# Performance work log

Hardware: AMD Instinct MI355X
Metric: run time of the kernel (lower is better)

## Reference

```python
import jax, jax.numpy as jnp
import numpy as np

KS = 3          # kernel size (forced by the view() shape constraint)
STRIDE = 1
PAD = 1
DIL = 1
K = KS * KS     # 9 taps


def _bilinear_sample(x, py, px):
    """x: [B,C,Hin,Win]; py,px: [B,C,K,H,W] float sample coords.
    Zero padding outside bounds (torchvision DeformConv semantics:
    each corner contributes only if it lies inside the image)."""
    B, C, Hin, Win = x.shape
    y0 = jnp.floor(py)
    x0 = jnp.floor(px)
    wy1 = py - y0
    wx1 = px - x0
    wy0 = 1.0 - wy1
    wx0 = 1.0 - wx1
    xf = x.reshape(B, C, Hin * Win)

    def gather(yi, xi):
        valid = (yi >= 0) & (yi <= Hin - 1) & (xi >= 0) & (xi <= Win - 1)
        yc = jnp.clip(yi, 0, Hin - 1).astype(jnp.int32)
        xc = jnp.clip(xi, 0, Win - 1).astype(jnp.int32)
        flat = (yc * Win + xc).reshape(B, C, -1)
        g = jnp.take_along_axis(xf, flat, axis=2).reshape(yi.shape)
        return jnp.where(valid, g, 0.0)

    return (wy0 * wx0 * gather(y0, x0)
            + wy0 * wx1 * gather(y0, x0 + 1)
            + wy1 * wx0 * gather(y0 + 1, x0)
            + wy1 * wx1 * gather(y0 + 1, x0 + 1))


def setup_inputs() -> dict:
    key = jax.random.key(0)
    ks = jax.random.split(key, 5)
    B, C, H, W = 8, 64, 128, 128
    Cout = 64
    return {
        "x": jax.random.normal(ks[0], (B, C, H, W), dtype=jnp.float32),
        # depthwise offset conv: groups=C, out = 18*C -> weight (18C, 1, 3, 3)
        "offset_w": jax.random.normal(ks[1], (2 * K * C, 1, 3, 3), dtype=jnp.float32) * 0.05,
        "offset_b": jax.random.normal(ks[2], (2 * K * C,), dtype=jnp.float32) * 0.05,
        "deform_w": jax.random.normal(ks[3], (Cout, C, KS, KS), dtype=jnp.float32) * 0.05,
        "deform_b": jax.random.normal(ks[4], (Cout,), dtype=jnp.float32) * 0.05,
    }


def reference(x, offset_w, offset_b, deform_w, deform_b):
    B, C, H, W = x.shape
    Cout = deform_w.shape[0]

    # 1) depthwise offset conv (groups = in_channels)
    off = jax.lax.conv_general_dilated(
        x, offset_w, window_strides=(STRIDE, STRIDE),
        padding=((PAD, PAD), (PAD, PAD)), rhs_dilation=(DIL, DIL),
        feature_group_count=C,
        dimension_numbers=("NCHW", "OIHW", "NCHW"))
    off = off + offset_b[None, :, None, None]

    # 2) softmax over the full channel axis (dim=1 in torch)
    off = jax.nn.softmax(off, axis=1)

    # 3) torchvision offset layout: channel 2*(g*K + k) + {0:dy, 1:dx},
    #    deformable_groups = C (per-input-channel offsets)
    off = off.reshape(B, C, K, 2, H, W)
    dy = off[:, :, :, 0]   # [B,C,K,H,W]
    dx = off[:, :, :, 1]

    base_y = (jnp.arange(H, dtype=x.dtype) * STRIDE - PAD)   # [H]
    base_x = (jnp.arange(W, dtype=x.dtype) * STRIDE - PAD)   # [W]
    ky = (jnp.repeat(jnp.arange(KS), KS) * DIL).astype(x.dtype)  # [K]
    kx = (jnp.tile(jnp.arange(KS), KS) * DIL).astype(x.dtype)

    py = base_y[None, None, None, :, None] + ky[None, None, :, None, None] + dy
    px = base_x[None, None, None, None, :] + kx[None, None, :, None, None] + dx

    sampled = _bilinear_sample(x, py, px)                    # [B,C,K,H,W]

    # 4) weighted accumulation over (c_in, kernel tap)
    out = jnp.einsum("bckhw,ock->bohw", sampled, deform_w.reshape(Cout, C, K))
    return out + deform_b[None, :, None, None]
```

## Files before the change

kernel.cpp:

```cpp
#include <hip/hip_runtime.h>

#define B_    8
#define C_    64
#define H_    128
#define W_    128
#define K_    9
#define J_    18
#define COUT_ 64
#define TPX   16
#define CK    576
#define SROW  584

typedef __attribute__((ext_vector_type(8))) short short8;
typedef __attribute__((ext_vector_type(4))) float float4v;

__device__ __forceinline__ unsigned short f2bf(float f) {
    unsigned int u = __float_as_uint(f);
    u = u + 0x7fffu + ((u >> 16) & 1u);
    return (unsigned short)(u >> 16);
}

constexpr int TMAP[9] = {0, 1, 2, 7, 8, 9, 14, 15, 16};

__global__ __launch_bounds__(256)
void nchw_to_nhwc(const float* __restrict__ x, float* __restrict__ xt) {
    __shared__ float tile[64][65];
    const int bid = blockIdx.x;
    const int wt  = bid & 1;
    const int h   = (bid >> 1) & 127;
    const int b   = bid >> 8;
    const int w0  = wt << 6;
    const int q   = threadIdx.x >> 6;
    const int l   = threadIdx.x & 63;
    #pragma unroll
    for (int r = 0; r < 16; r++) {
        const int c = q * 16 + r;
        tile[c][l] = x[((size_t)(b * C_ + c) * H_ + h) * W_ + w0 + l];
    }
    __syncthreads();
    #pragma unroll
    for (int r = 0; r < 16; r++) {
        const int w = q * 16 + r;
        xt[((size_t)(b * H_ + h) * W_ + w0 + w) * C_ + l] = tile[l][w];
    }
}

__global__ __launch_bounds__(256)
void conv_dw_bf16(const float* __restrict__ dw, unsigned short* __restrict__ dwb) {
    const int i = blockIdx.x * 256 + threadIdx.x;
    if (i < CK * COUT_) dwb[i] = f2bf(dw[i]);
}

template<int T>
__device__ __forceinline__ void conv_steps(const unsigned int* __restrict__ owc,
                                           const float (&S)[28], float (&v)[4][J_]) {
    if constexpr (T < 81) {
        const unsigned int pw = owc[T];
        const float wlo = __uint_as_float(pw << 16);
        const float whi = __uint_as_float(pw & 0xffff0000u);
        constexpr int e0 = 2 * T, e1 = 2 * T + 1;
        constexpr int j0 = e0 / 9, p0 = TMAP[e0 % 9];
        constexpr int j1 = e1 / 9, p1 = TMAP[e1 % 9];
        #pragma unroll
        for (int px = 0; px < 4; px++) {
            v[px][j0] = fmaf(wlo, S[p0 + px], v[px][j0]);
            v[px][j1] = fmaf(whi, S[p1 + px], v[px][j1]);
        }
        conv_steps<T + 1>(owc, S, v);
    }
}

template<int I>
__device__ __forceinline__ void finish_px(float (&v)[J_], const float (&S)[28],
                                          unsigned short* __restrict__ sb) {
    float sum = 0.0f;
    #pragma unroll
    for (int j = 0; j < J_; j++) { v[j] = __expf(v[j]); sum += v[j]; }
    #pragma unroll
    for (int off = 32; off >= 1; off >>= 1) sum += __shfl_xor(sum, off, 64);
    const float inv = 1.0f / sum;
    #pragma unroll
    for (int k = 0; k < K_; k++) {
        const float dy = v[2 * k] * inv;
        const float dx = v[2 * k + 1] * inv;
        const int base = TMAP[k] + I;
        const float a  = S[base],     bb = S[base + 1];
        const float c  = S[base + 7], dd = S[base + 8];
        const float top = a + dx * (bb - a);
        const float bot = c + dx * (dd - c);
        sb[k] = f2bf(top + dy * (bot - top));
    }
}

template<bool NHWC, bool PREB>
__global__ __launch_bounds__(256, 3)
void dcn_fused(const float* __restrict__ xsrc,
               const float* __restrict__ ow,
               const float* __restrict__ ob,
               const float* __restrict__ dw,
               const unsigned short* __restrict__ dwb,
               const float* __restrict__ db,
               float* __restrict__ out) {
    __shared__ unsigned int ow_s[C_ * 81];
    __shared__ __align__(16) unsigned short sbuf[TPX * SROW];

    const int tid  = threadIdx.x;
    const int wave = tid >> 6;
    const int lane = tid & 63;

    const int bid = blockIdx.x;
    const int b   = bid >> 10;
    const int rem = bid & 1023;
    const int h   = rem >> 3;
    const int w0  = (rem & 7) << 4;

    const float2* ow2 = (const float2*)ow;
    for (int i = tid; i < C_ * 81; i += 256) {
        float2 f = ow2[i];
        ow_s[i] = (unsigned int)f2bf(f.x) | ((unsigned int)f2bf(f.y) << 16);
    }

    __syncthreads();

    const int wbase = w0 + (wave << 2);
    const unsigned int* owc = ow_s + lane * 81;
    const float2* obp = (const float2*)(ob + lane * J_);

    float S[28];
    #pragma unroll
    for (int r = 0; r < 4; r++) {
        const int y = h - 1 + r;
        const bool yv = (unsigned)y < (unsigned)H_;
        #pragma unroll
        for (int s = 0; s < 7; s++) {
            const int xx = wbase - 1 + s;
            const bool ok = yv && ((unsigned)xx < (unsigned)W_);
            float val;
            if (NHWC) {
                const float* p = xsrc + ((size_t)(b * H_ + (y & 127)) * W_ + (xx & 127)) * C_ + lane;
                val = ok ? *p : 0.0f;
            } else {
                const float* p = xsrc + ((size_t)(b * C_ + lane) * H_ + (y & 127)) * W_ + (xx & 127);
                val = ok ? *p : 0.0f;
            }
            S[r * 7 + s] = val;
        }
    }

    float v[4][J_];
    #pragma unroll
    for (int p = 0; p < 9; p++) {
        const float2 f = obp[p];
        #pragma unroll
        for (int px = 0; px < 4; px++) { v[px][2 * p] = f.x; v[px][2 * p + 1] = f.y; }
    }
    conv_steps<0>(owc, S, v);

    unsigned short* sb = sbuf + (wave << 2) * SROW + lane * K_;
    finish_px<0>(v[0], S, sb);
    finish_px<1>(v[1], S, sb + SROW);
    finish_px<2>(v[2], S, sb + 2 * SROW);
    finish_px<3>(v[3], S, sb + 3 * SROW);

    __syncthreads();

    const int quad = lane >> 4;
    const int o    = (wave << 4) + (lane & 15);
    float4v acc = {0.f, 0.f, 0.f, 0.f};
    const unsigned short* arow = sbuf + (lane & 15) * SROW + quad * 8;
    #pragma unroll
    for (int t = 0; t < 18; t++) {
        short8 afrag = *(const short8*)(arow + t * 32);
        short8 bfrag;
        if (PREB) {
            bfrag = *(const short8*)(dwb + (size_t)o * CK + quad * 8 + t * 32);
        } else {
            const float* brow = dw + (size_t)o * CK + quad * 8 + t * 32;
            float4 b0 = *(const float4*)brow;
            float4 b1 = *(const float4*)(brow + 4);
            union { short8 s8; unsigned short u[8]; } bfu;
            bfu.u[0] = f2bf(b0.x); bfu.u[1] = f2bf(b0.y); bfu.u[2] = f2bf(b0.z); bfu.u[3] = f2bf(b0.w);
            bfu.u[4] = f2bf(b1.x); bfu.u[5] = f2bf(b1.y); bfu.u[6] = f2bf(b1.z); bfu.u[7] = f2bf(b1.w);
            bfrag = bfu.s8;
        }
        acc = __builtin_amdgcn_mfma_f32_16x16x32_bf16(afrag, bfrag, acc, 0, 0, 0);
    }
    const float bias = db[o];
    const int px0 = quad << 2;
    float4 res;
    res.x = acc[0] + bias; res.y = acc[1] + bias; res.z = acc[2] + bias; res.w = acc[3] + bias;
    *(float4*)(out + ((size_t)(b * COUT_ + o) * H_ + h) * W_ + w0 + px0) = res;
}

extern "C" void kernel_launch(void* const* d_in, const int* in_sizes, int n_in,
                              void* d_out, int out_size, void* d_ws, size_t ws_size,
                              hipStream_t stream) {
    (void)in_sizes; (void)n_in; (void)out_size;
    const float* x  = (const float*)d_in[0];
    const float* ow = (const float*)d_in[1];
    const float* ob = (const float*)d_in[2];
    const float* dw = (const float*)d_in[3];
    const float* db = (const float*)d_in[4];
    float* outp = (float*)d_out;

    const size_t xbytes  = (size_t)B_ * C_ * H_ * W_ * sizeof(float);
    const size_t dwbytes = (size_t)CK * COUT_ * sizeof(unsigned short);
    const dim3 grid(B_ * H_ * (W_ / TPX)), blk(256);

    if (ws_size >= xbytes + dwbytes) {
        float* xt = (float*)d_ws;
        unsigned short* dwb = (unsigned short*)((char*)d_ws + xbytes);
        nchw_to_nhwc<<<dim3(B_ * H_ * (W_ / 64)), blk, 0, stream>>>(x, xt);
        conv_dw_bf16<<<dim3((CK * COUT_ + 255) / 256), blk, 0, stream>>>(dw, dwb);
        dcn_fused<true, true><<<grid, blk, 0, stream>>>(xt, ow, ob, dw, dwb, db, outp);
    } else if (ws_size >= xbytes) {
        float* xt = (float*)d_ws;
        nchw_to_nhwc<<<dim3(B_ * H_ * (W_ / 64)), blk, 0, stream>>>(x, xt);
        dcn_fused<true, false><<<grid, blk, 0, stream>>>(xt, ow, ob, dw, nullptr, db, outp);
    } else {
        dcn_fused<false, false><<<grid, blk, 0, stream>>>(x, ow, ob, dw, nullptr, db, outp);
    }
}
```

Measured before the change: 206.0 us.

## Prepack offset weights, alias LDS buffers, use packed FMA and exp2 softmax

Offset-conv weights are now repacked once in a prep kernel into a dy/dx-paired bf16 layout, pre-scaled by log2(e), so each block copies them into LDS instead of converting them. The shared weight buffer and the bf16 tap buffer now alias one LDS allocation, which cuts LDS per block and may allow more resident blocks. The offset conv uses packed two-wide FMAs, exp becomes exp2, and the reciprocal uses the hardware rcp. The cross-lane sum uses ds_swizzle for four pixels at once, and a fast path skips bounds checks for interior windows. It adds a barrier before the LDS reuse and slightly less accurate exp and reciprocal.

```diff
diff --git a/kernel.cpp b/kernel.cpp
--- a/kernel.cpp
+++ b/kernel.cpp
@@ -10,9 +10,12 @@
 #define TPX   16
 #define CK    576
 #define SROW  584
+#define NW81  (C_ * 81)
+#define L2E   1.4426950408889634f
 
 typedef __attribute__((ext_vector_type(8))) short short8;
 typedef __attribute__((ext_vector_type(4))) float float4v;
+typedef __attribute__((ext_vector_type(2))) float f32x2;
 
 __device__ __forceinline__ unsigned short f2bf(float f) {
     unsigned int u = __float_as_uint(f);
@@ -46,63 +49,74 @@
 }
 
 __global__ __launch_bounds__(256)
-void conv_dw_bf16(const float* __restrict__ dw, unsigned short* __restrict__ dwb) {
-    const int i = blockIdx.x * 256 + threadIdx.x;
-    if (i < CK * COUT_) dwb[i] = f2bf(dw[i]);
+void prep_weights(const float* __restrict__ dw, unsigned short* __restrict__ dwb,
+                  const float* __restrict__ ow, unsigned int* __restrict__ owp) {
+    const int bid = blockIdx.x;
+    const int dwblocks = (CK * COUT_) / 256;
+    if (bid < dwblocks) {
+        const int i = bid * 256 + threadIdx.x;
+        dwb[i] = f2bf(dw[i]);
+    } else {
+        const int i = (bid - dwblocks) * 256 + threadIdx.x;
+        if (i < NW81) {
+            const int c = i / 81, r = i - c * 81;
+            const int k = r / 9,  t = r - k * 9;
+            const float* s = ow + c * 162 + k * 18 + t;
+            owp[i] = (unsigned int)f2bf(s[0] * L2E) |
+                     ((unsigned int)f2bf(s[9] * L2E) << 16);
+        }
+    }
 }
 
 template<int T>
 __device__ __forceinline__ void conv_steps(const unsigned int* __restrict__ owc,
-                                           const float (&S)[28], float (&v)[4][J_]) {
+                                           const float (&S)[28], f32x2 (&v2)[4][9]) {
     if constexpr (T < 81) {
         const unsigned int pw = owc[T];
-        const float wlo = __uint_as_float(pw << 16);
-        const float whi = __uint_as_float(pw & 0xffff0000u);
-        constexpr int e0 = 2 * T, e1 = 2 * T + 1;
-        constexpr int j0 = e0 / 9, p0 = TMAP[e0 % 9];
-        constexpr int j1 = e1 / 9, p1 = TMAP[e1 % 9];
+        const f32x2 w2 = {__uint_as_float(pw << 16),
+                          __uint_as_float(pw & 0xffff0000u)};
+        constexpr int k = T / 9;
+        constexpr int p = TMAP[T % 9];
         #pragma unroll
         for (int px = 0; px < 4; px++) {
-            v[px][j0] = fmaf(wlo, S[p0 + px], v[px][j0]);
-            v[px][j1] = fmaf(whi, S[p1 + px], v[px][j1]);
-        }
-        conv_steps<T + 1>(owc, S, v);
+            const float s = S[p + px];
+            v2[px][k] = __builtin_elementwise_fma(w2, (f32x2){s, s}, v2[px][k]);
+        }
+        conv_steps<T + 1>(owc, S, v2);
     }
 }
 
 template<int I>
-__device__ __forceinline__ void finish_px(float (&v)[J_], const float (&S)[28],
-                                          unsigned short* __restrict__ sb) {
-    float sum = 0.0f;
-    #pragma unroll
-    for (int j = 0; j < J_; j++) { v[j] = __expf(v[j]); sum += v[j]; }
-    #pragma unroll
-    for (int off = 32; off >= 1; off >>= 1) sum += __shfl_xor(sum, off, 64);
-    const float inv = 1.0f / sum;
-    #pragma unroll
-    for (int k = 0; k < K_; k++) {
-        const float dy = v[2 * k] * inv;
-        const float dx = v[2 * k + 1] * inv;
+__device__ __forceinline__ void taps_px(const f32x2 (&w)[9], const float inv,
+                                        const float (&S)[28],
+                                        unsigned short* __restrict__ sb) {
+    #pragma unroll
+    for (int k = 0; k < 9; k++) {
+        const float dy = w[k].x * inv;
+        const float dx = w[k].y * inv;
         const int base = TMAP[k] + I;
         const float a  = S[base],     bb = S[base + 1];
         const float c  = S[base + 7], dd = S[base + 8];
-        const float top = a + dx * (bb - a);
-        const float bot = c + dx * (dd - c);
-        sb[k] = f2bf(top + dy * (bot - top));
-    }
-}
-
-template<bool NHWC, bool PREB>
+        const float top = fmaf(dx, bb - a, a);
+        const float bot = fmaf(dx, dd - c, c);
+        sb[k] = f2bf(fmaf(dy, bot - top, top));
+    }
+}
+
+template<bool NHWC, bool PREB, bool PREP>
 __global__ __launch_bounds__(256, 3)
 void dcn_fused(const float* __restrict__ xsrc,
                const float* __restrict__ ow,
+               const unsigned int* __restrict__ owp,
                const float* __restrict__ ob,
                const float* __restrict__ dw,
                const unsigned short* __restrict__ dwb,
                const float* __restrict__ db,
                float* __restrict__ out) {
-    __shared__ unsigned int ow_s[C_ * 81];
-    __shared__ __align__(16) unsigned short sbuf[TPX * SROW];
+    static_assert(TPX * SROW * sizeof(unsigned short) <= NW81 * sizeof(unsigned int), "union");
+    __shared__ __align__(16) unsigned int smem[NW81];
+    unsigned int* ow_s = smem;
+    unsigned short* sbuf = (unsigned short*)smem;
 
     const int tid  = threadIdx.x;
     const int wave = tid >> 6;
@@ -114,53 +128,108 @@
     const int h   = rem >> 3;
     const int w0  = (rem & 7) << 4;
 
-    const float2* ow2 = (const float2*)ow;
-    for (int i = tid; i < C_ * 81; i += 256) {
-        float2 f = ow2[i];
-        ow_s[i] = (unsigned int)f2bf(f.x) | ((unsigned int)f2bf(f.y) << 16);
-    }
-
+    if (PREP) {
+        #pragma unroll
+        for (int i = 0; i < 21; i++) {
+            const int idx = tid + i * 256;
+            if (idx < NW81) ow_s[idx] = owp[idx];
+        }
+    } else {
+        for (int i = tid; i < NW81; i += 256) {
+            const int c = i / 81, r = i - c * 81;
+            const int k = r / 9,  t = r - k * 9;
+            const float* s = ow + c * 162 + k * 18 + t;
+            ow_s[i] = (unsigned int)f2bf(s[0] * L2E) |
+                      ((unsigned int)f2bf(s[9] * L2E) << 16);
+        }
+    }
     __syncthreads();
 
     const int wbase = w0 + (wave << 2);
     const unsigned int* owc = ow_s + lane * 81;
+
+    float S[28];
+    if (h >= 1 && h <= H_ - 3 && wbase >= 1 && wbase <= W_ - 6) {
+        const float* p0 = NHWC
+            ? xsrc + ((size_t)(b * H_ + (h - 1)) * W_ + (wbase - 1)) * C_ + lane
+            : xsrc + ((size_t)(b * C_ + lane) * H_ + (h - 1)) * W_ + (wbase - 1);
+        const int rs = NHWC ? (W_ * C_) : W_;
+        const int cs = NHWC ? C_ : 1;
+        #pragma unroll
+        for (int r = 0; r < 4; r++)
+            #pragma unroll
+            for (int s = 0; s < 7; s++)
+                S[r * 7 + s] = p0[r * rs + s * cs];
+    } else {
+        #pragma unroll
+        for (int r = 0; r < 4; r++) {
+            const int y = h - 1 + r;
+            const bool yv = (unsigned)y < (unsigned)H_;
+            #pragma unroll
+            for (int s = 0; s < 7; s++) {
+                const int xx = wbase - 1 + s;
+                const bool ok = yv && ((unsigned)xx < (unsigned)W_);
+                const float* p = NHWC
+                    ? xsrc + ((size_t)(b * H_ + (y & 127)) * W_ + (xx & 127)) * C_ + lane
+                    : xsrc + ((size_t)(b * C_ + lane) * H_ + (y & 127)) * W_ + (xx & 127);
+                S[r * 7 + s] = ok ? *p : 0.0f;
+            }
+        }
+    }
+
+    f32x2 v2[4][9];
     const float2* obp = (const float2*)(ob + lane * J_);
-
-    float S[28];
-    #pragma unroll
-    for (int r = 0; r < 4; r++) {
-        const int y = h - 1 + r;
-        const bool yv = (unsigned)y < (unsigned)H_;
-        #pragma unroll
-        for (int s = 0; s < 7; s++) {
-            const int xx = wbase - 1 + s;
-            const bool ok = yv && ((unsigned)xx < (unsigned)W_);
-            float val;
-            if (NHWC) {
-                const float* p = xsrc + ((size_t)(b * H_ + (y & 127)) * W_ + (xx & 127)) * C_ + lane;
-                val = ok ? *p : 0.0f;
-            } else {
-                const float* p = xsrc + ((size_t)(b * C_ + lane) * H_ + (y & 127)) * W_ + (xx & 127);
-                val = ok ? *p : 0.0f;
-            }
-            S[r * 7 + s] = val;
-        }
-    }
-
-    float v[4][J_];
     #pragma unroll
     for (int p = 0; p < 9; p++) {
         const float2 f = obp[p];
-        #pragma unroll
-        for (int px = 0; px < 4; px++) { v[px][2 * p] = f.x; v[px][2 * p + 1] = f.y; }
-    }
-    conv_steps<0>(owc, S, v);
+        const f32x2 b2 = {f.x * L2E, f.y * L2E};
+        v2[0][p] = b2; v2[1][p] = b2; v2[2][p] = b2; v2[3][p] = b2;
+    }
+    conv_steps<0>(owc, S, v2);
+
+    float psum[4];
+    #pragma unroll
+    for (int px = 0; px < 4; px++) {
+        float s = 0.0f;
+        #pragma unroll
+        for (int k = 0; k < 9; k++) {
+            f32x2 e;
+            e.x = __builtin_amdgcn_exp2f(v2[px][k].x);
+            e.y = __builtin_amdgcn_exp2f(v2[px][k].y);
+            v2[px][k] = e;
+            s += e.x + e.y;
+        }
+        psum[px] = s;
+    }
+
+    __syncthreads();
+
+    #pragma unroll
+    for (int px = 0; px < 4; px++) psum[px] += __shfl_xor(psum[px], 32, 64);
+#define RED_LEVEL(PAT) do { \
+        const float r0_ = __uint_as_float((unsigned)__builtin_amdgcn_ds_swizzle((int)__float_as_uint(psum[0]), (PAT))); \
+        const float r1_ = __uint_as_float((unsigned)__builtin_amdgcn_ds_swizzle((int)__float_as_uint(psum[1]), (PAT))); \
+        const float r2_ = __uint_as_float((unsigned)__builtin_amdgcn_ds_swizzle((int)__float_as_uint(psum[2]), (PAT))); \
+        const float r3_ = __uint_as_float((unsigned)__builtin_amdgcn_ds_swizzle((int)__float_as_uint(psum[3]), (PAT))); \
+        psum[0] += r0_; psum[1] += r1_; psum[2] += r2_; psum[3] += r3_; \
+    } while (0)
+    RED_LEVEL(0x401F);
+    RED_LEVEL(0x201F);
+    RED_LEVEL(0x101F);
+    RED_LEVEL(0x081F);
+    RED_LEVEL(0x041F);
+#undef RED_LEVEL
+
+    const float inv0 = __builtin_amdgcn_rcpf(psum[0]);
+    const float inv1 = __builtin_amdgcn_rcpf(psum[1]);
+    const float inv2 = __builtin_amdgcn_rcpf(psum[2]);
+    const float inv3 = __builtin_amdgcn_rcpf(psum[3]);
 
     unsigned short* sb = sbuf + (wave << 2) * SROW + lane * K_;
-    finish_px<0>(v[0], S, sb);
-    finish_px<1>(v[1], S, sb + SROW);
-    finish_px<2>(v[2], S, sb + 2 * SROW);
-    finish_px<3>(v[3], S, sb + 3 * SROW);
+    taps_px<0>(v2[0], inv0, S, sb);
+    taps_px<1>(v2[1], inv1, S, sb + SROW);
+    taps_px<2>(v2[2], inv2, S, sb + 2 * SROW);
+    taps_px<3>(v2[3], inv3, S, sb + 3 * SROW);
 
     __syncthreads();
 
@@ -205,19 +274,29 @@
 
     const size_t xbytes  = (size_t)B_ * C_ * H_ * W_ * sizeof(float);
     const size_t dwbytes = (size_t)CK * COUT_ * sizeof(unsigned short);
+    const size_t owbytes = (size_t)NW81 * sizeof(unsigned int);
     const dim3 grid(B_ * H_ * (W_ / TPX)), blk(256);
-
-    if (ws_size >= xbytes + dwbytes) {
+    const int dwblocks = (CK * COUT_) / 256;
+    const int owblocks = (NW81 + 255) / 256;
+
+    if (ws_size >= xbytes + dwbytes + owbytes) {
         float* xt = (float*)d_ws;
         unsigned short* dwb = (unsigned short*)((char*)d_ws + xbytes);
-        nchw_to_nhwc<<<dim3(B_ * H_ * (W_ / 64)), blk, 0, stream>>>(x, xt);
-        conv_dw_bf16<<<dim3((CK * COUT_ + 255) / 256), blk, 0, stream>>>(dw, dwb);
-        dcn_fused<true, true><<<grid, blk, 0, stream>>>(xt, ow, ob, dw, dwb, db, outp);
+        unsigned int* owp = (unsigned int*)((char*)d_ws + xbytes + dwbytes);
+        nchw_to_nhwc<<<dim3(B_ * H_ * 2), blk, 0, stream>>>(x, xt);
+        prep_weights<<<dim3(dwblocks + owblocks), blk, 0, stream>>>(dw, dwb, ow, owp);
+        dcn_fused<true, true, true><<<grid, blk, 0, stream>>>(xt, ow, owp, ob, dw, dwb, db, outp);
+    } else if (ws_size >= xbytes + dwbytes) {
+        float* xt = (float*)d_ws;
+        unsigned short* dwb = (unsigned short*)((char*)d_ws + xbytes);
+        nchw_to_nhwc<<<dim3(B_ * H_ * 2), blk, 0, stream>>>(x, xt);
+        prep_weights<<<dim3(dwblocks), blk, 0, stream>>>(dw, dwb, nullptr, nullptr);
+        dcn_fused<true, true, false><<<grid, blk, 0, stream>>>(xt, ow, nullptr, ob, dw, dwb, db, outp);
     } else if (ws_size >= xbytes) {
         float* xt = (float*)d_ws;
-        nchw_to_nhwc<<<dim3(B_ * H_ * (W_ / 64)), blk, 0, stream>>>(x, xt);
-        dcn_fused<true, false><<<grid, blk, 0, stream>>>(xt, ow, ob, dw, nullptr, db, outp);
+        nchw_to_nhwc<<<dim3(B_ * H_ * 2), blk, 0, stream>>>(x, xt);
+        dcn_fused<true, false, false><<<grid, blk, 0, stream>>>(xt, ow, nullptr, ob, dw, nullptr, db, outp);
     } else {
-        dcn_fused<false, false><<<grid, blk, 0, stream>>>(x, ow, ob, dw, nullptr, db, outp);
-    }
-}
+        dcn_fused<false, false, false><<<grid, blk, 0, stream>>>(x, ow, nullptr, ob, dw, nullptr, db, outp);
+    }
+}
```

Result: faster. 201.6 us (-2.2%).
